# Performance work log

Measured on AMD Instinct MI355X. Metric: run time of the kernel, lower is better.

Reference implementation:

```python
import jax, jax.numpy as jnp
import numpy as np

B, D, M, P, I, O = 256, 10, 32, 36, 8, 16
NUM_ITERATIONS = 3
EPS = 1e-07


def squash(s, axis=-1):
    sq = jnp.sum(s * s, axis=axis, keepdims=True)
    safe_norm = jnp.sqrt(sq + EPS)
    scale = sq / (1.0 + sq)
    return scale * (s / safe_norm)


def setup_inputs() -> dict:
    key = jax.random.key(0)
    kx, kw = jax.random.split(key)
    x = jax.random.normal(kx, (B, M, P, I), dtype=jnp.float32)
    # Parameter shape matches torch: [1, D, M, 1, O, I]
    W = 0.01 * jax.random.normal(kw, (1, D, M, 1, O, I), dtype=jnp.float32)
    return {"x": x, "W": W}


def reference(x, W):
    Wd = W[0, :, :, 0]  # [D, M, O, I]
    # u_hat: [B, D, M, P, O]
    u_hat = jnp.einsum('dmoi,bmpi->bdmpo', Wd, x)
    tu = jax.lax.stop_gradient(u_hat)
    b = jnp.zeros(u_hat.shape[:4], dtype=u_hat.dtype)  # [B, D, M, P]
    for _ in range(NUM_ITERATIONS - 1):
        c = jax.nn.softmax(b, axis=1)                 # over digit caps
        s = jnp.einsum('bdmp,bdmpo->bdo', c, tu)
        v = squash(s)
        b = b + jnp.einsum('bdmpo,bdo->bdmp', tu, v)
    # Final softmax over dim=3 (primary-cap axis), faithful to source
    c = jax.nn.softmax(b, axis=3)
    s = jnp.einsum('bdmp,bdmpo->bdo', c, u_hat)
    return squash(s)
```

## Files before the change

### kernel.cpp

```cpp
#include <hip/hip_runtime.h>
#include <math.h>

#define BB 256
#define DD 10
#define MM 32
#define PP 36
#define II 8
#define OO 16
#define NT 640
#define XS 292
#define RS 37

__device__ __forceinline__ float dot8(const float4 a0, const float4 a1,
                                      const float4 b0, const float4 b1) {
    return a0.x*b0.x + a0.y*b0.y + a0.z*b0.z + a0.w*b0.w
         + a1.x*b1.x + a1.y*b1.y + a1.z*b1.z + a1.w*b1.w;
}
__device__ __forceinline__ float dot4(const float4 a, const float4 b) {
    return a.x*b.x + a.y*b.y + a.z*b.z + a.w*b.w;
}

__global__ void __launch_bounds__(NT, 3) caps_routing(
    const float* __restrict__ x,
    const float* __restrict__ W,
    float* __restrict__ out)
{
    const int bidx = blockIdx.x;
    const int tid  = threadIdx.x;
    const int wave = tid >> 6;
    const int lane = tid & 63;
    const float* __restrict__ xb = x + (size_t)bidx * (MM*PP*II);

    __shared__ __align__(16) float xs  [MM*XS];
    __shared__ __align__(16) float z   [DD*MM*II];
    __shared__ __align__(16) float y   [DD*MM*II];
    __shared__ __align__(16) float ybar[MM*II];
    __shared__ __align__(16) float rinv[MM*RS];

    {
        const float4* xg = (const float4*)xb;
        #pragma unroll
        for (int k = 0; k < 4; ++k) {
            const int t = tid + k*NT;
            if (t < MM*72) {
                const int m = t / 72, r = t - m*72;
                *(float4*)(xs + m*XS + 4*r) = xg[t];
            }
        }
        if (tid < MM*II) {
            const int m = tid >> 3, i = tid & 7;
            const float* xr = xb + m*(PP*II) + i;
            float acc = 0.f;
            #pragma unroll 6
            for (int p = 0; p < PP; ++p) acc += xr[p*II];
            ybar[tid] = 0.1f * acc;
        }
    }
    __syncthreads();

    {
        const int d = wave;
        const int o = lane & 15, q = lane >> 4;
        float s1 = 0.f;
        #pragma unroll
        for (int j = 0; j < 8; ++j) {
            const int m = q*8 + j;
            const float4* wp = (const float4*)(W + ((size_t)((d*MM + m)*OO + o)) * II);
            const float4* yp = (const float4*)(ybar + m*II);
            s1 += dot8(wp[0], wp[1], yp[0], yp[1]);
        }
        s1 += __shfl_xor(s1, 16, 64);
        s1 += __shfl_xor(s1, 32, 64);
        float sq = s1 * s1;
        sq += __shfl_xor(sq, 1, 64);
        sq += __shfl_xor(sq, 2, 64);
        sq += __shfl_xor(sq, 4, 64);
        sq += __shfl_xor(sq, 8, 64);
        const float v1 = (sq / (1.f + sq)) * (s1 / sqrtf(sq + 1e-7f));
        float vv[OO];
        #pragma unroll
        for (int o2 = 0; o2 < OO; ++o2) vv[o2] = __shfl(v1, o2, 64);

        const int mz = lane >> 1, ihz = lane & 1;
        const float* wz = W + ((size_t)(d*MM + mz)*OO) * II + ihz*4;
        float a0 = 0.f, a1 = 0.f, a2 = 0.f, a3 = 0.f;
        #pragma unroll
        for (int o2 = 0; o2 < OO; ++o2) {
            const float4 wv = *(const float4*)(wz + o2*II);
            a0 += wv.x * vv[o2]; a1 += wv.y * vv[o2];
            a2 += wv.z * vv[o2]; a3 += wv.w * vv[o2];
        }
        *(float4*)(z + (d*MM + mz)*II + ihz*4) = make_float4(a0, a1, a2, a3);
    }
    __syncthreads();

    #pragma unroll
    for (int k = 0; k < 2; ++k) {
        const int t = tid + k*NT;
        if (t < MM*PP) {
            const int m = t / PP, p = t - m*PP;
            const float4* xp = (const float4*)(xs + m*XS + p*II);
            const float4 x0 = xp[0], x1 = xp[1];
            float se = 0.f;
            #pragma unroll
            for (int d2 = 0; d2 < DD; ++d2) {
                const float4* zp = (const float4*)(z + (d2*MM + m)*II);
                se += __expf(dot8(x0, x1, zp[0], zp[1]));
            }
            rinv[m*RS + p] = 1.0f / se;
        }
    }
    __syncthreads();

    {
        const int d = wave;
        const float* __restrict__ zd = z + d*(MM*II);
        float* __restrict__ yd = y + d*(MM*II);

        const int mL = lane >> 1, ih = lane & 1;
        const float* xr = xs + mL*XS + ih*4;
        const float4 zh = *(const float4*)(zd + mL*II + ih*4);

        {
            const float* rr = rinv + mL*RS;
            float a0=0.f, a1=0.f, a2=0.f, a3=0.f;
            #pragma unroll 6
            for (int p = 0; p < PP; ++p) {
                const float4 xh = *(const float4*)(xr + p*II);
                float bh = dot4(xh, zh);
                bh += __shfl_xor(bh, 1, 64);
                const float e = __expf(bh) * rr[p];
                a0 += e*xh.x; a1 += e*xh.y; a2 += e*xh.z; a3 += e*xh.w;
            }
            *(float4*)(yd + mL*II + ih*4) = make_float4(a0,a1,a2,a3);
        }

        const int o = lane & 15, q = lane >> 4;
        float s2 = 0.f;
        #pragma unroll
        for (int j = 0; j < 8; ++j) {
            const int m = q*8 + j;
            const float4* wp = (const float4*)(W + ((size_t)((d*MM + m)*OO + o)) * II);
            const float4* yp = (const float4*)(yd + m*II);
            s2 += dot8(wp[0], wp[1], yp[0], yp[1]);
        }
        s2 += __shfl_xor(s2, 16, 64);
        s2 += __shfl_xor(s2, 32, 64);
        float sq = s2 * s2;
        sq += __shfl_xor(sq, 1, 64);
        sq += __shfl_xor(sq, 2, 64);
        sq += __shfl_xor(sq, 4, 64);
        sq += __shfl_xor(sq, 8, 64);
        const float v2 = (sq / (1.f + sq)) * (s2 / sqrtf(sq + 1e-7f));
        float vv[OO];
        #pragma unroll
        for (int o2 = 0; o2 < OO; ++o2) vv[o2] = __shfl(v2, o2, 64);

        float4 zh2;
        {
            const float* wz = W + ((size_t)(d*MM + mL)*OO) * II + ih*4;
            float a0 = 0.f, a1 = 0.f, a2 = 0.f, a3 = 0.f;
            #pragma unroll
            for (int o2 = 0; o2 < OO; ++o2) {
                const float4 wv = *(const float4*)(wz + o2*II);
                a0 += wv.x * vv[o2]; a1 += wv.y * vv[o2];
                a2 += wv.z * vv[o2]; a3 += wv.w * vv[o2];
            }
            zh2 = make_float4(zh.x + a0, zh.y + a1, zh.z + a2, zh.w + a3);
        }

        {
            float se = 0.f;
            float a0=0.f, a1=0.f, a2=0.f, a3=0.f;
            #pragma unroll 6
            for (int p = 0; p < PP; ++p) {
                const float4 xh = *(const float4*)(xr + p*II);
                float bh = dot4(xh, zh2);
                bh += __shfl_xor(bh, 1, 64);
                const float e = __expf(bh);
                se += e;
                a0 += e*xh.x; a1 += e*xh.y; a2 += e*xh.z; a3 += e*xh.w;
            }
            const float rs = 1.f / se;
            *(float4*)(yd + mL*II + ih*4) = make_float4(a0*rs, a1*rs, a2*rs, a3*rs);
        }

        float s3 = 0.f;
        #pragma unroll
        for (int j = 0; j < 8; ++j) {
            const int m = q*8 + j;
            const float4* wp = (const float4*)(W + ((size_t)((d*MM + m)*OO + o)) * II);
            const float4* yp = (const float4*)(yd + m*II);
            s3 += dot8(wp[0], wp[1], yp[0], yp[1]);
        }
        s3 += __shfl_xor(s3, 16, 64);
        s3 += __shfl_xor(s3, 32, 64);
        float sq3 = s3 * s3;
        sq3 += __shfl_xor(sq3, 1, 64);
        sq3 += __shfl_xor(sq3, 2, 64);
        sq3 += __shfl_xor(sq3, 4, 64);
        sq3 += __shfl_xor(sq3, 8, 64);
        const float r = (sq3 / (1.f + sq3)) * (s3 / sqrtf(sq3 + 1e-7f));
        if (lane < OO)
            out[(size_t)bidx * (DD*OO) + d*OO + o] = r;
    }
}

extern "C" void kernel_launch(void* const* d_in, const int* in_sizes, int n_in,
                              void* d_out, int out_size, void* d_ws, size_t ws_size,
                              hipStream_t stream) {
    (void)in_sizes; (void)n_in; (void)out_size; (void)d_ws; (void)ws_size;
    const float* x = (const float*)d_in[0];
    const float* W = (const float*)d_in[1];
    float* out = (float*)d_out;
    caps_routing<<<dim3(BB), dim3(NT), 0, stream>>>(x, W, out);
}
```

Before: 78.05 us.

## Split routing loops over p-halves per lane and broadcast v via LDS

The per-wave routing loops are remapped so each lane owns a full 8-wide input row for one m and half of the p range, instead of half of the i dimension over all p. This removes the per-iteration cross-lane shuffle inside the exp loops and replaces it with one shuffle reduction across the two p-halves after the loop. The z update now splits the o dimension across the halves in the same way. The 16 shuffles that broadcast v are replaced by a write to shared memory followed by float4 reads. The cost is more accumulator registers and more shuffles after each loop, and the v broadcast relies on wavefront-synchronous LDS visibility with no explicit barrier.

```diff
diff --git a/kernel.cpp b/kernel.cpp
--- a/kernel.cpp
+++ b/kernel.cpp
@@ -5,6 +5,7 @@
 #define DD 10
 #define MM 32
 #define PP 36
+#define PH (PP/2)
 #define II 8
 #define OO 16
 #define NT 640
@@ -15,9 +16,6 @@
                                       const float4 b0, const float4 b1) {
     return a0.x*b0.x + a0.y*b0.y + a0.z*b0.z + a0.w*b0.w
          + a1.x*b1.x + a1.y*b1.y + a1.z*b1.z + a1.w*b1.w;
-}
-__device__ __forceinline__ float dot4(const float4 a, const float4 b) {
-    return a.x*b.x + a.y*b.y + a.z*b.z + a.w*b.w;
 }
 
 __global__ void __launch_bounds__(NT, 3) caps_routing(
@@ -36,6 +34,7 @@
     __shared__ __align__(16) float y   [DD*MM*II];
     __shared__ __align__(16) float ybar[MM*II];
     __shared__ __align__(16) float rinv[MM*RS];
+    __shared__ __align__(16) float v_l [DD*OO];
 
     {
         const float4* xg = (const float4*)xb;
@@ -60,11 +59,11 @@
 
     {
         const int d = wave;
-        const int o = lane & 15, q = lane >> 4;
+        const int o = lane & 15, qq = lane >> 4;
         float s1 = 0.f;
         #pragma unroll
         for (int j = 0; j < 8; ++j) {
-            const int m = q*8 + j;
+            const int m = qq*8 + j;
             const float4* wp = (const float4*)(W + ((size_t)((d*MM + m)*OO + o)) * II);
             const float4* yp = (const float4*)(ybar + m*II);
             s1 += dot8(wp[0], wp[1], yp[0], yp[1]);
@@ -77,18 +76,22 @@
         sq += __shfl_xor(sq, 4, 64);
         sq += __shfl_xor(sq, 8, 64);
         const float v1 = (sq / (1.f + sq)) * (s1 / sqrtf(sq + 1e-7f));
-        float vv[OO];
-        #pragma unroll
-        for (int o2 = 0; o2 < OO; ++o2) vv[o2] = __shfl(v1, o2, 64);
-
+        if (lane < OO) v_l[d*OO + lane] = v1;
+
+        const float4 vv0 = *(const float4*)(v_l + d*OO);
+        const float4 vv1 = *(const float4*)(v_l + d*OO + 4);
+        const float4 vv2 = *(const float4*)(v_l + d*OO + 8);
+        const float4 vv3 = *(const float4*)(v_l + d*OO + 12);
+        const float vs[16] = {vv0.x,vv0.y,vv0.z,vv0.w, vv1.x,vv1.y,vv1.z,vv1.w,
+                              vv2.x,vv2.y,vv2.z,vv2.w, vv3.x,vv3.y,vv3.z,vv3.w};
         const int mz = lane >> 1, ihz = lane & 1;
         const float* wz = W + ((size_t)(d*MM + mz)*OO) * II + ihz*4;
         float a0 = 0.f, a1 = 0.f, a2 = 0.f, a3 = 0.f;
         #pragma unroll
         for (int o2 = 0; o2 < OO; ++o2) {
             const float4 wv = *(const float4*)(wz + o2*II);
-            a0 += wv.x * vv[o2]; a1 += wv.y * vv[o2];
-            a2 += wv.z * vv[o2]; a3 += wv.w * vv[o2];
+            a0 += wv.x * vs[o2]; a1 += wv.y * vs[o2];
+            a2 += wv.z * vs[o2]; a3 += wv.w * vs[o2];
         }
         *(float4*)(z + (d*MM + mz)*II + ihz*4) = make_float4(a0, a1, a2, a3);
     }
@@ -117,29 +120,36 @@
         const float* __restrict__ zd = z + d*(MM*II);
         float* __restrict__ yd = y + d*(MM*II);
 
-        const int mL = lane >> 1, ih = lane & 1;
-        const float* xr = xs + mL*XS + ih*4;
-        const float4 zh = *(const float4*)(zd + mL*II + ih*4);
+        const int mF = lane & 31;
+        const int ph = lane >> 5;
+        const float* xr = xs + mF*XS + (ph*PH)*II;
+        const float4 zf0 = *(const float4*)(zd + mF*II);
+        const float4 zf1 = *(const float4*)(zd + mF*II + 4);
 
         {
-            const float* rr = rinv + mL*RS;
-            float a0=0.f, a1=0.f, a2=0.f, a3=0.f;
+            const float* rr = rinv + mF*RS + ph*PH;
+            float a0=0.f,a1=0.f,a2=0.f,a3=0.f,a4=0.f,a5=0.f,a6=0.f,a7=0.f;
             #pragma unroll 6
-            for (int p = 0; p < PP; ++p) {
-                const float4 xh = *(const float4*)(xr + p*II);
-                float bh = dot4(xh, zh);
-                bh += __shfl_xor(bh, 1, 64);
-                const float e = __expf(bh) * rr[p];
-                a0 += e*xh.x; a1 += e*xh.y; a2 += e*xh.z; a3 += e*xh.w;
-            }
-            *(float4*)(yd + mL*II + ih*4) = make_float4(a0,a1,a2,a3);
-        }
-
-        const int o = lane & 15, q = lane >> 4;
+            for (int q = 0; q < PH; ++q) {
+                const float4 x0 = *(const float4*)(xr + q*II);
+                const float4 x1 = *(const float4*)(xr + q*II + 4);
+                const float e = __expf(dot8(x0, x1, zf0, zf1)) * rr[q];
+                a0 += e*x0.x; a1 += e*x0.y; a2 += e*x0.z; a3 += e*x0.w;
+                a4 += e*x1.x; a5 += e*x1.y; a6 += e*x1.z; a7 += e*x1.w;
+            }
+            a0 += __shfl_xor(a0, 32, 64); a1 += __shfl_xor(a1, 32, 64);
+            a2 += __shfl_xor(a2, 32, 64); a3 += __shfl_xor(a3, 32, 64);
+            a4 += __shfl_xor(a4, 32, 64); a5 += __shfl_xor(a5, 32, 64);
+            a6 += __shfl_xor(a6, 32, 64); a7 += __shfl_xor(a7, 32, 64);
+            const float4 wv = ph ? make_float4(a4,a5,a6,a7) : make_float4(a0,a1,a2,a3);
+            *(float4*)(yd + mF*II + ph*4) = wv;
+        }
+
+        const int o = lane & 15, qq = lane >> 4;
         float s2 = 0.f;
         #pragma unroll
         for (int j = 0; j < 8; ++j) {
-            const int m = q*8 + j;
+            const int m = qq*8 + j;
             const float4* wp = (const float4*)(W + ((size_t)((d*MM + m)*OO + o)) * II);
             const float4* yp = (const float4*)(yd + m*II);
             s2 += dot8(wp[0], wp[1], yp[0], yp[1]);
@@ -152,43 +162,62 @@
         sq += __shfl_xor(sq, 4, 64);
         sq += __shfl_xor(sq, 8, 64);
         const float v2 = (sq / (1.f + sq)) * (s2 / sqrtf(sq + 1e-7f));
-        float vv[OO];
-        #pragma unroll
-        for (int o2 = 0; o2 < OO; ++o2) vv[o2] = __shfl(v2, o2, 64);
-
-        float4 zh2;
+        if (lane < OO) v_l[d*OO + lane] = v2;
+        const float4 vv0 = *(const float4*)(v_l + d*OO);
+        const float4 vv1 = *(const float4*)(v_l + d*OO + 4);
+        const float4 vv2 = *(const float4*)(v_l + d*OO + 8);
+        const float4 vv3 = *(const float4*)(v_l + d*OO + 12);
+        const float vs[16] = {vv0.x,vv0.y,vv0.z,vv0.w, vv1.x,vv1.y,vv1.z,vv1.w,
+                              vv2.x,vv2.y,vv2.z,vv2.w, vv3.x,vv3.y,vv3.z,vv3.w};
+
+        float4 zf20, zf21;
         {
-            const float* wz = W + ((size_t)(d*MM + mL)*OO) * II + ih*4;
-            float a0 = 0.f, a1 = 0.f, a2 = 0.f, a3 = 0.f;
+            const float* wz = W + ((size_t)(d*MM + mF)*OO) * II;
+            float b0=0.f,b1=0.f,b2=0.f,b3=0.f,b4=0.f,b5=0.f,b6=0.f,b7=0.f;
             #pragma unroll
-            for (int o2 = 0; o2 < OO; ++o2) {
-                const float4 wv = *(const float4*)(wz + o2*II);
-                a0 += wv.x * vv[o2]; a1 += wv.y * vv[o2];
-                a2 += wv.z * vv[o2]; a3 += wv.w * vv[o2];
-            }
-            zh2 = make_float4(zh.x + a0, zh.y + a1, zh.z + a2, zh.w + a3);
+            for (int j = 0; j < 8; ++j) {
+                const int o2 = ph*8 + j;
+                const float4 w0 = *(const float4*)(wz + o2*II);
+                const float4 w1 = *(const float4*)(wz + o2*II + 4);
+                const float s = vs[o2];
+                b0 += w0.x*s; b1 += w0.y*s; b2 += w0.z*s; b3 += w0.w*s;
+                b4 += w1.x*s; b5 += w1.y*s; b6 += w1.z*s; b7 += w1.w*s;
+            }
+            b0 += __shfl_xor(b0, 32, 64); b1 += __shfl_xor(b1, 32, 64);
+            b2 += __shfl_xor(b2, 32, 64); b3 += __shfl_xor(b3, 32, 64);
+            b4 += __shfl_xor(b4, 32, 64); b5 += __shfl_xor(b5, 32, 64);
+            b6 += __shfl_xor(b6, 32, 64); b7 += __shfl_xor(b7, 32, 64);
+            zf20 = make_float4(zf0.x + b0, zf0.y + b1, zf0.z + b2, zf0.w + b3);
+            zf21 = make_float4(zf1.x + b4, zf1.y + b5, zf1.z + b6, zf1.w + b7);
         }
 
         {
             float se = 0.f;
-            float a0=0.f, a1=0.f, a2=0.f, a3=0.f;
+            float a0=0.f,a1=0.f,a2=0.f,a3=0.f,a4=0.f,a5=0.f,a6=0.f,a7=0.f;
             #pragma unroll 6
-            for (int p = 0; p < PP; ++p) {
-                const float4 xh = *(const float4*)(xr + p*II);
-                float bh = dot4(xh, zh2);
-                bh += __shfl_xor(bh, 1, 64);
-                const float e = __expf(bh);
+            for (int q = 0; q < PH; ++q) {
+                const float4 x0 = *(const float4*)(xr + q*II);
+                const float4 x1 = *(const float4*)(xr + q*II + 4);
+                const float e = __expf(dot8(x0, x1, zf20, zf21));
                 se += e;
-                a0 += e*xh.x; a1 += e*xh.y; a2 += e*xh.z; a3 += e*xh.w;
-            }
+                a0 += e*x0.x; a1 += e*x0.y; a2 += e*x0.z; a3 += e*x0.w;
+                a4 += e*x1.x; a5 += e*x1.y; a6 += e*x1.z; a7 += e*x1.w;
+            }
+            se += __shfl_xor(se, 32, 64);
+            a0 += __shfl_xor(a0, 32, 64); a1 += __shfl_xor(a1, 32, 64);
+            a2 += __shfl_xor(a2, 32, 64); a3 += __shfl_xor(a3, 32, 64);
+            a4 += __shfl_xor(a4, 32, 64); a5 += __shfl_xor(a5, 32, 64);
+            a6 += __shfl_xor(a6, 32, 64); a7 += __shfl_xor(a7, 32, 64);
             const float rs = 1.f / se;
-            *(float4*)(yd + mL*II + ih*4) = make_float4(a0*rs, a1*rs, a2*rs, a3*rs);
+            const float4 wv = ph ? make_float4(a4*rs,a5*rs,a6*rs,a7*rs)
+                                 : make_float4(a0*rs,a1*rs,a2*rs,a3*rs);
+            *(float4*)(yd + mF*II + ph*4) = wv;
         }
 
         float s3 = 0.f;
         #pragma unroll
         for (int j = 0; j < 8; ++j) {
-            const int m = q*8 + j;
+            const int m = qq*8 + j;
             const float4* wp = (const float4*)(W + ((size_t)((d*MM + m)*OO + o)) * II);
             const float4* yp = (const float4*)(yd + m*II);
             s3 += dot8(wp[0], wp[1], yp[0], yp[1]);
```

After: 78.68 us. About the same (+0.8%).
